# Kernel optimization log

Hardware: AMD Instinct MI355X
Metric: run time of the kernel (lower is better)

The kernel has to match this reference:

```python
import jax, jax.numpy as jnp
import numpy as np

N_ATOMS = 10000
N_PAIRS = 100000
H = 64          # hidden_channels
R = 32          # number_of_radial_basis_functions
MAX_Z = 100
CUTOFF = 0.5    # nm (radial_max_distance), min = 0.0


def cosine_cutoff(d):
    # 0.5*(cos(pi*d/rc)+1) for d < rc else 0
    return jnp.where(d < CUTOFF, 0.5 * (jnp.cos(jnp.pi * d / CUTOFF) + 1.0), 0.0)


def expnormal_rbf(d):
    # ExpNormal smearing (TorchMD/TensorNet style), cutoff_lower = 0
    start = float(np.exp(-CUTOFF))
    means = jnp.linspace(start, 1.0, R, dtype=d.dtype)            # [R]
    beta = (2.0 / R * (1.0 - start)) ** -2
    alpha = 5.0 / CUTOFF
    return jnp.exp(-beta * (jnp.exp(-alpha * d)[:, None] - means) ** 2)  # [P,R]


def vector_to_skewtensor(v):
    x, y, z = v[:, 0], v[:, 1], v[:, 2]
    o = jnp.zeros_like(x)
    return jnp.stack([o, -z, y, z, o, -x, -y, x, o], axis=-1).reshape(-1, 3, 3)


def vector_to_symtensor(v):
    t = v[:, :, None] * v[:, None, :]                              # [P,3,3]
    tr3 = (t[:, 0, 0] + t[:, 1, 1] + t[:, 2, 2]) / 3.0
    return t - tr3[:, None, None] * jnp.eye(3, dtype=v.dtype)


def setup_inputs() -> dict:
    key = jax.random.key(0)
    ks = jax.random.split(key, 20)
    atomic_numbers = jax.random.randint(ks[0], (N_ATOMS,), 0, MAX_Z)
    pair_indices = jax.random.randint(ks[1], (2, N_PAIRS), 0, N_ATOMS)
    r_ij = jax.random.normal(ks[2], (N_PAIRS, 3), dtype=jnp.float32) * 0.12  # ~0.2 nm norms
    d_ij = jnp.linalg.norm(r_ij, axis=-1, keepdims=True) + 1e-6
    s = 0.1
    p = {
        'emb':    jax.random.normal(ks[3], (MAX_Z, H)) * s,
        'emb2_w': jax.random.normal(ks[4], (H, 2 * H)) * s,
        'emb2_b': jnp.zeros((H,)),
        'dp1_w':  jax.random.normal(ks[5], (H, R)) * s,
        'dp1_b':  jnp.zeros((H,)),
        'dp2_w':  jax.random.normal(ks[6], (H, R)) * s,
        'dp2_b':  jnp.zeros((H,)),
        'dp3_w':  jax.random.normal(ks[7], (H, R)) * s,
        'dp3_b':  jnp.zeros((H,)),
        'lt0_w':  jax.random.normal(ks[8], (H, H)) * s,
        'lt1_w':  jax.random.normal(ks[9], (H, H)) * s,
        'lt2_w':  jax.random.normal(ks[10], (H, H)) * s,
        'ls1_w':  jax.random.normal(ks[11], (2 * H, H)) * s,
        'ls1_b':  jnp.zeros((2 * H,)),
        'ls2_w':  jax.random.normal(ks[12], (3 * H, 2 * H)) * s,
        'ls2_b':  jnp.zeros((3 * H,)),
        'ln_g':   jnp.ones((H,)),
        'ln_b':   jnp.zeros((H,)),
    }
    return dict(atomic_numbers=atomic_numbers, pair_indices=pair_indices,
                d_ij=d_ij, r_ij=r_ij, **p)


def reference(atomic_numbers, pair_indices, d_ij, r_ij,
              emb, emb2_w, emb2_b, dp1_w, dp1_b, dp2_w, dp2_b, dp3_w, dp3_b,
              lt0_w, lt1_w, lt2_w, ls1_w, ls1_b, ls2_w, ls2_b, ln_g, ln_b):
    n_atoms = atomic_numbers.shape[0]
    src = pair_indices[0]
    # atomic number message Zij: concat(emb[i], emb[j]) -> Linear
    zi = emb[atomic_numbers]                                      # [N,H]
    zij = jnp.concatenate([zi[src], zi[pair_indices[1]]], axis=-1)  # [P,2H]
    Zij = zij @ emb2_w.T + emb2_b                                 # [P,H]
    d = d_ij[:, 0]                                                # [P]
    unit = r_ij / d_ij                                            # [P,3]
    rc = cosine_cutoff(d)                                         # [P]
    rbf = expnormal_rbf(d) * rc[:, None]                          # [P,R]
    C = rc[:, None] * Zij                                         # [P,H]
    f1 = (rbf @ dp1_w.T + dp1_b) * C                              # [P,H]
    f2 = (rbf @ dp2_w.T + dp2_b) * C * 10.0                       # Angstrom scale
    f3 = (rbf @ dp3_w.T + dp3_b) * C * 100.0
    eye = jnp.eye(3, dtype=r_ij.dtype)
    skew = vector_to_skewtensor(unit)                             # [P,3,3]
    sym = vector_to_symtensor(unit)                               # [P,3,3]
    Iij = f1[:, :, None, None] * eye                              # [P,H,3,3]
    Aij = f2[:, :, None, None] * skew[:, None]
    Sij = f3[:, :, None, None] * sym[:, None]
    I = jax.ops.segment_sum(Iij, src, num_segments=n_atoms)       # [N,H,3,3]
    A = jax.ops.segment_sum(Aij, src, num_segments=n_atoms)
    S = jax.ops.segment_sum(Sij, src, num_segments=n_atoms)
    # tensor_norm -> LayerNorm -> scalar MLP
    tn = jnp.sum((I + A + S) ** 2, axis=(-2, -1))                 # [N,H]
    mu = tn.mean(-1, keepdims=True)
    var = tn.var(-1, keepdims=True)
    norm = (tn - mu) / jnp.sqrt(var + 1e-5) * ln_g + ln_b
    norm = jax.nn.silu(norm @ ls1_w.T + ls1_b)
    norm = jax.nn.silu(norm @ ls2_w.T + ls2_b)                    # [N,3H]
    norm = norm.reshape(-1, H, 3)
    I = jnp.einsum('nhij,gh->ngij', I, lt0_w) * norm[:, :, 0][:, :, None, None]
    A = jnp.einsum('nhij,gh->ngij', A, lt1_w) * norm[:, :, 1][:, :, None, None]
    S = jnp.einsum('nhij,gh->ngij', S, lt2_w) * norm[:, :, 2][:, :, None, None]
    return I + A + S
```

## Files before the change

### kernel.cpp

```cpp
#include <hip/hip_runtime.h>
#include <hip/hip_bf16.h>

#define N_ATOMS 10000
#define N_PAIRS 100000
#define HH 64
#define MAXZ 100

typedef _Float16 h2_t __attribute__((ext_vector_type(2)));

constexpr float RBF_START = 0.6065306597126334f;
constexpr float RBF_STEP  = (1.0f - RBF_START) / 31.0f;
constexpr float RBF_BETA  = 1.0f / ((0.0625f * (1.0f - RBF_START)) * (0.0625f * (1.0f - RBF_START)));
constexpr float LOG2E     = 1.4426950408889634f;
constexpr float NEG_ALPHA_L2 = -10.0f * LOG2E;
constexpr float NEG_BETA_L2  = -RBF_BETA * LOG2E;

#define OFF_EMB   0
#define OFF_W2    6400
#define OFF_B2    14592
#define OFF_D1W   14656
#define OFF_D1B   16704
#define OFF_D2W   16768
#define OFF_D2B   18816
#define OFF_D3W   18880
#define OFF_D3B   20928
#define OFF_LT0   20992
#define OFF_LT1   25088
#define OFF_LT2   29184
#define OFF_L1W   33280
#define OFF_L1B   41472
#define OFF_L2W   41600
#define OFF_L2B   66176
#define OFF_LNG   66368
#define OFF_LNB   66432
#define N_PARAMF  66496

#define PH_DP   0
#define PH_L1   3072
#define PH_L2   7168
#define PH_LT   19456
#define PH_N    25600

#define WS_WF     0
#define WS_CNT    266240
#define WS_OFF    307200
#define WS_CUR    348160
#define WS_T1     389120
#define WS_T2     414720
#define WS_PH     440320
#define WS_DPK    542720
#define WS_ZNL    2142720
#define WS_ACCH   2542720

__device__ __forceinline__ float bf2f(unsigned short u) {
    return __uint_as_float(((unsigned int)u) << 16);
}
__device__ __forceinline__ float fexp2(float x) { return __builtin_amdgcn_exp2f(x); }
__device__ __forceinline__ float fcos2pi(float x) { return __builtin_amdgcn_cosf(x); }
__device__ __forceinline__ float fsilu(float x) { return x / (1.0f + fexp2(-LOG2E * x)); }
__device__ __forceinline__ h2_t u2h(unsigned u) { return __builtin_bit_cast(h2_t, u); }
__device__ __forceinline__ unsigned packh2(float a, float b) {
    h2_t v; v.x = (_Float16)a; v.y = (_Float16)b;
    return __builtin_bit_cast(unsigned, v);
}

#if __has_builtin(__builtin_amdgcn_fdot2)
__device__ __forceinline__ float FDOT2(h2_t a, h2_t b, float c) {
    return __builtin_amdgcn_fdot2(a, b, c, false);
}
#else
__device__ __forceinline__ float FDOT2(h2_t a, h2_t b, float c) {
    return c + (float)a.x * (float)b.x + (float)a.y * (float)b.y;
}
#endif
__device__ __forceinline__ float dot16v(uint4 a, uint4 b, float acc) {
    acc = FDOT2(u2h(a.x), u2h(b.x), acc);
    acc = FDOT2(u2h(a.y), u2h(b.y), acc);
    acc = FDOT2(u2h(a.z), u2h(b.z), acc);
    acc = FDOT2(u2h(a.w), u2h(b.w), acc);
    return acc;
}
__device__ __forceinline__ float dot16h(const uint4* w, const uint4* x, float acc) {
    return dot16v(*w, *x, acc);
}

__device__ int classify64(const unsigned short* b, int lane) {
    unsigned short x = b[lane];
    int e = (x >> 7) & 0xFF;
    bool implaus = (x != 0) && (e < 96 || e > 133);
    bool zeroeven = ((lane & 1) == 0) && (x == 0);
    unsigned long long mi = __ballot(implaus);
    unsigned long long mz = __ballot(zeroeven);
    if (__popcll(mz) == 32) return 0;
    if (__popcll(mi) >= 8) return 0;
    return 1;
}

struct ConvArgs { const void* src[18]; float* dst; };

__global__ void k_prep(ConvArgs a, const int* __restrict__ pidx, int* __restrict__ cnt) {
    const int sizes[18] = {6400,8192,64,2048,64,2048,64,2048,64,4096,4096,4096,8192,128,24576,192,64,64};
    __shared__ int fl;
    if (threadIdx.x < 64) {
        int f = classify64((const unsigned short*)a.src[0], threadIdx.x);
        if (threadIdx.x == 0) fl = f;
    }
    __syncthreads();
    int t = blockIdx.x * 256 + threadIdx.x;
    if (t < N_PARAMF) {
        int acc = 0, seg = 0, off = t;
        #pragma unroll
        for (int i = 0; i < 18; ++i) {
            if (t >= acc && t < acc + sizes[i]) { seg = i; off = t - acc; }
            acc += sizes[i];
        }
        if (fl == 1) a.dst[t] = bf2f(((const unsigned short*)a.src[seg])[off]);
        else         a.dst[t] = ((const float*)a.src[seg])[off];
    }
    if (t < N_PAIRS) atomicAdd(&cnt[pidx[t]], 1);
}

__global__ void k_scantab(const float* __restrict__ WF, float* __restrict__ T1,
                          float* __restrict__ T2, unsigned* __restrict__ PH,
                          const int* __restrict__ cnt, int* __restrict__ offs,
                          int* __restrict__ cur) {
    __shared__ int buf[1024];
    if (blockIdx.x == 0) {
        int tid = threadIdx.x;
        int base = tid * 10;
        int c[10]; int s = 0;
        #pragma unroll
        for (int i = 0; i < 10; ++i) {
            int idx = base + i;
            int v = (idx < N_ATOMS) ? cnt[idx] : 0;
            c[i] = v; s += v;
        }
        buf[tid] = s;
        __syncthreads();
        for (int off = 1; off < 1024; off <<= 1) {
            int v = (tid >= off) ? buf[tid - off] : 0;
            __syncthreads();
            buf[tid] += v;
            __syncthreads();
        }
        int run = buf[tid] - s;
        #pragma unroll
        for (int i = 0; i < 10; ++i) {
            int idx = base + i;
            if (idx < N_ATOMS) { offs[idx] = run; cur[idx] = run; run += c[i]; }
        }
        if (tid == 0) offs[N_ATOMS] = N_PAIRS;
        return;
    }
    int t = (blockIdx.x - 1) * 1024 + threadIdx.x;
    if (t < 6400) {
        int z = t >> 6, h = t & 63;
        const float* ez = WF + OFF_EMB + z * HH;
        const float* w2 = WF + OFF_W2 + h * 128;
        float s1 = 0.f, s2 = 0.f;
        #pragma unroll
        for (int k = 0; k < 64; ++k) {
            float e = ez[k];
            s1 += w2[k] * e;
            s2 += w2[64 + k] * e;
        }
        T1[z * HH + h] = s1;
        T2[z * HH + h] = s2;
    }
    if (t < PH_N) {
        int src;
        if (t < PH_L1) {
            int w = t >> 10, r = t & 1023;
            src = (w == 0 ? OFF_D1W : (w == 1 ? OFF_D2W : OFF_D3W)) + r * 2;
        } else if (t < PH_L2) {
            src = OFF_L1W + (t - PH_L1) * 2;
        } else if (t < PH_LT) {
            src = OFF_L2W + (t - PH_L2) * 2;
        } else {
            src = OFF_LT0 + (t - PH_LT) * 2;
        }
        PH[t] = packh2(WF[src], WF[src + 1]);
    }
}

__global__ void k_fill(const int* __restrict__ pidx, const int* __restrict__ an,
                       const void* __restrict__ dij_v, const void* __restrict__ rij_v,
                       int* __restrict__ cur,
                       float4* __restrict__ dpack, int* __restrict__ znl) {
    __shared__ int fdr[2];
    if (threadIdx.x < 64) {
        int fd = classify64((const unsigned short*)dij_v, threadIdx.x);
        int fr = classify64((const unsigned short*)rij_v, threadIdx.x);
        if (threadIdx.x == 0) { fdr[0] = fd; fdr[1] = fr; }
    }
    __syncthreads();
    int p = blockIdx.x * 256 + threadIdx.x;
    if (p >= N_PAIRS) return;
    int s = pidx[p];
    int dst = pidx[N_PAIRS + p];
    int pos = atomicAdd(&cur[s], 1);
    float d, rx, ry, rz;
    if (fdr[0] == 1) d = bf2f(((const unsigned short*)dij_v)[p]);
    else             d = ((const float*)dij_v)[p];
    if (fdr[1] == 1) {
        const unsigned short* r = (const unsigned short*)rij_v;
        rx = bf2f(r[3*p]); ry = bf2f(r[3*p+1]); rz = bf2f(r[3*p+2]);
    } else {
        const float* r = (const float*)rij_v;
        rx = r[3*p]; ry = r[3*p+1]; rz = r[3*p+2];
    }
    float inv = 1.0f / d;
    dpack[pos] = make_float4(rx * inv, ry * inv, rz * inv, d);
    znl[pos] = an[dst];
}

__global__ __launch_bounds__(256, 2) void k_pair(
    const int* __restrict__ an,
    const float* __restrict__ WF,
    const int* __restrict__ offs,
    const float4* __restrict__ dpack, const int* __restrict__ znl,
    const float* __restrict__ T1, const float* __restrict__ T2,
    const unsigned* __restrict__ PH,
    unsigned* __restrict__ accH)
{
    __shared__ __align__(16) unsigned rbuf[4][2][16];

    const int wave = threadIdx.x >> 6;
    const int h    = threadIdx.x & 63;

    const uint4* wp = (const uint4*)(PH + PH_DP);
    const uint4 w10 = wp[        h * 4 + 0], w11 = wp[        h * 4 + 1],
                w12 = wp[        h * 4 + 2], w13 = wp[        h * 4 + 3];
    const uint4 w20 = wp[256 +   h * 4 + 0], w21 = wp[256 +   h * 4 + 1],
                w22 = wp[256 +   h * 4 + 2], w23 = wp[256 +   h * 4 + 3];
    const uint4 w30 = wp[512 +   h * 4 + 0], w31 = wp[512 +   h * 4 + 1],
                w32 = wp[512 +   h * 4 + 2], w33 = wp[512 +   h * 4 + 3];

    const float ed1 = (WF + OFF_D1B)[h];
    const float ed2 = (WF + OFF_D2B)[h];
    const float ed3 = (WF + OFF_D3B)[h];
    const float eb2 = (WF + OFF_B2)[h];
    const float lng = (WF + OFF_LNG)[h];
    const float lnb = (WF + OFF_LNB)[h];

    unsigned* sl0 = &rbuf[wave][0][0];
    unsigned* sl1 = &rbuf[wave][1][0];
    const int stride = gridDim.x * 4;

    for (int n = blockIdx.x * 4 + wave; n < N_ATOMS; n += stride) {
        const float zA = eb2 + T1[an[n] * HH + h];
        const int pbeg = offs[n];
        const int len  = offs[n + 1] - pbeg;

        float Is=0.f, sx=0.f, sy=0.f, sz=0.f;
        float Sxx=0.f, Syy=0.f, Szz=0.f, Sxy=0.f, Sxz=0.f, Syz=0.f;

        float4 dc = make_float4(0,0,0,0), dn = make_float4(0,0,0,0);
        float tc = 0.f, t2n = 0.f, rc_c = 0.f, rc_n = 0.f;
        if (len > 0) { dc = dpack[pbeg];     tc  = T2[znl[pbeg] * HH + h]; }
        if (len > 1) { dn = dpack[pbeg + 1]; t2n = T2[znl[pbeg + 1] * HH + h]; }
        if (len > 0) {
            float d = dc.w;
            rc_c = (d < 0.5f) ? 0.5f * (fcos2pi(d) + 1.0f) : 0.0f;
            float en = fexp2(NEG_ALPHA_L2 * d);
            if (h < 16) {
                float t0 = en - (RBF_START + RBF_STEP * (float)(2 * h));
                float t1 = en - (RBF_START + RBF_STEP * (float)(2 * h + 1));
                sl0[h] = packh2(fexp2(NEG_BETA_L2 * t0 * t0) * rc_c,
                                fexp2(NEG_BETA_L2 * t1 * t1) * rc_c);
            }
        }
        __builtin_amdgcn_wave_barrier();

        for (int ii = 0; ii < len; ++ii) {
            if (ii + 1 < len) {
                float d = dn.w;
                rc_n = (d < 0.5f) ? 0.5f * (fcos2pi(d) + 1.0f) : 0.0f;
                float en = fexp2(NEG_ALPHA_L2 * d);
                unsigned* sl = (ii & 1) ? sl0 : sl1;
                if (h < 16) {
                    float t0 = en - (RBF_START + RBF_STEP * (float)(2 * h));
                    float t1 = en - (RBF_START + RBF_STEP * (float)(2 * h + 1));
                    sl[h] = packh2(fexp2(NEG_BETA_L2 * t0 * t0) * rc_n,
                                   fexp2(NEG_BETA_L2 * t1 * t1) * rc_n);
                }
            }
            float4 d2v = make_float4(0,0,0,0); float t2v2 = 0.f;
            bool has2 = (ii + 2 < len);
            if (has2) {
                d2v  = dpack[pbeg + ii + 2];
                t2v2 = T2[znl[pbeg + ii + 2] * HH + h];
            }
            const uint4* rbp = (const uint4*)((ii & 1) ? sl1 : sl0);
            uint4 b0 = rbp[0], b1 = rbp[1], b2 = rbp[2], b3 = rbp[3];
            float g1 = ed1, g2 = ed2, g3 = ed3;
            g1 = dot16v(w10, b0, g1); g1 = dot16v(w11, b1, g1);
            g1 = dot16v(w12, b2, g1); g1 = dot16v(w13, b3, g1);
            g2 = dot16v(w20, b0, g2); g2 = dot16v(w21, b1, g2);
            g2 = dot16v(w22, b2, g2); g2 = dot16v(w23, b3, g2);
            g3 = dot16v(w30, b0, g3); g3 = dot16v(w31, b1, g3);
            g3 = dot16v(w32, b2, g3); g3 = dot16v(w33, b3, g3);

            float ux = dc.x, uy = dc.y, uz = dc.z;
            float Cc = rc_c * (zA + tc);
            float f1 = g1 * Cc;
            float f2 = g2 * Cc * 10.0f;
            float f3 = g3 * Cc * 100.0f;

            Is += f1;
            sx += f2 * ux;  sy += f2 * uy;  sz += f2 * uz;
            float q = (ux*ux + uy*uy + uz*uz) * (1.0f / 3.0f);
            Sxx += f3 * (ux*ux - q);
            Syy += f3 * (uy*uy - q);
            Szz += f3 * (uz*uz - q);
            Sxy += f3 * (ux*uy);
            Sxz += f3 * (ux*uz);
            Syz += f3 * (uy*uz);

            dc = dn; tc = t2n; rc_c = rc_n;
            if (has2) { dn = d2v; t2n = t2v2; }
            __builtin_amdgcn_wave_barrier();
        }

        float tn = 3.0f*Is*Is + 2.0f*(sx*sx + sy*sy + sz*sz)
                 + Sxx*Sxx + Syy*Syy + Szz*Szz
                 + 2.0f*(Sxy*Sxy + Sxz*Sxz + Syz*Syz);
        float s1 = tn, s2 = tn * tn;
        #pragma unroll
        for (int o = 32; o > 0; o >>= 1) {
            s1 += __shfl_xor(s1, o);
            s2 += __shfl_xor(s2, o);
        }
        float mu  = s1 * (1.0f / 64.0f);
        float var = s2 * (1.0f / 64.0f) - mu * mu;
        float nv  = (tn - mu) * rsqrtf(var + 1e-5f) * lng + lnb;

        float vals[11] = {Is, sx, sy, sz, Sxx, Syy, Szz, Sxy, Sxz, Syz, nv};
        #pragma unroll
        for (int c = 0; c < 11; ++c) {
            float pv = __shfl_xor(vals[c], 1);
            if ((h & 1) == 0)
                accH[((n * 11 + c) << 5) + (h >> 1)] = packh2(vals[c], pv);
        }
    }
}

__global__ __launch_bounds__(256, 2) void k_post(
    const float* __restrict__ WF,
    const unsigned* __restrict__ PH,
    const unsigned* __restrict__ accH,
    float* __restrict__ out)
{
    __shared__ __align__(16) unsigned wL2[192 * 68];
    __shared__ __align__(16) unsigned acch[4][12 * 32];
    __shared__ __align__(16) unsigned y1h[4][64];
    __shared__ __align__(16) unsigned y2h[4][96];

    for (int q = threadIdx.x; q < 12288; q += 256) {
        int m = q >> 6, u = q & 63;
        wL2[m * 68 + u] = PH[PH_L2 + q];
    }
    __syncthreads();

    const int wave = threadIdx.x >> 6;
    const int h    = threadIdx.x & 63;
    const int gw   = blockIdx.x * 4 + wave;
    const int GW   = gridDim.x * 4;

    const uint4* l1base = (const uint4*)(PH + PH_L1);
    const uint4* lt0 = (const uint4*)(PH + PH_LT) + h * 8;
    const uint4* lt1 = (const uint4*)(PH + PH_LT + 2048) + h * 8;
    const uint4* lt2 = (const uint4*)(PH + PH_LT + 4096) + h * 8;

    for (int n = gw; n < N_ATOMS; n += GW) {
        if (h < 32) {
            #pragma unroll
            for (int c = 0; c < 11; ++c)
                acch[wave][c * 32 + h] = accH[((n * 11 + c) << 5) + h];
        }
        __builtin_amdgcn_wave_barrier();

        const uint4* nvh = (const uint4*)&acch[wave][10 * 32];

        float ya = (WF + OFF_L1B)[h];
        float yb = (WF + OFF_L1B)[h + 64];
        {
            const uint4* ra = l1base + h * 8;
            const uint4* rb = l1base + (h + 64) * 8;
            #pragma unroll
            for (int k = 0; k < 8; ++k) {
                ya = dot16h(ra + k, nvh + k, ya);
                yb = dot16h(rb + k, nvh + k, yb);
            }
        }
        ya = fsilu(ya); yb = fsilu(yb);
        {
            float pa = __shfl_xor(ya, 1);
            float pb = __shfl_xor(yb, 1);
            if ((h & 1) == 0) {
                y1h[wave][(h >> 1)]      = packh2(ya, pa);
                y1h[wave][32 + (h >> 1)] = packh2(yb, pb);
            }
        }
        __builtin_amdgcn_wave_barrier();

        const uint4* y1p = (const uint4*)&y1h[wave][0];
        float z0 = (WF + OFF_L2B)[h];
        float z1 = (WF + OFF_L2B)[h + 64];
        float z2 = (WF + OFF_L2B)[h + 128];
        {
            const uint4* r0 = (const uint4*)&wL2[(h)       * 68];
            const uint4* r1 = (const uint4*)&wL2[(h + 64)  * 68];
            const uint4* r2 = (const uint4*)&wL2[(h + 128) * 68];
            #pragma unroll
            for (int k = 0; k < 16; ++k) {
                uint4 x = y1p[k];
                z0 = dot16v(r0[k], x, z0);
                z1 = dot16v(r1[k], x, z1);
                z2 = dot16v(r2[k], x, z2);
            }
        }
        z0 = fsilu(z0); z1 = fsilu(z1); z2 = fsilu(z2);
        {
            float p0 = __shfl_xor(z0, 1);
            float p1 = __shfl_xor(z1, 1);
            float p2 = __shfl_xor(z2, 1);
            if ((h & 1) == 0) {
                y2h[wave][(h >> 1)]      = packh2(z0, p0);
                y2h[wave][32 + (h >> 1)] = packh2(z1, p1);
                y2h[wave][64 + (h >> 1)] = packh2(z2, p2);
            }
        }
        __builtin_amdgcn_wave_barrier();

        float n0, n1, n2;
        {
            int i0 = 3 * h;
            unsigned u0 = y2h[wave][i0 >> 1];
            unsigned u1 = y2h[wave][(i0 >> 1) + 1];
            h2_t a = u2h(u0), b = u2h(u1);
            if (i0 & 1) { n0 = (float)a.y; n1 = (float)b.x; n2 = (float)b.y; }
            else        { n0 = (float)a.x; n1 = (float)a.y; n2 = (float)b.x; }
        }

        const uint4* aI  = (const uint4*)&acch[wave][0];
        const uint4* aAx = (const uint4*)&acch[wave][32];
        const uint4* aAy = (const uint4*)&acch[wave][64];
        const uint4* aAz = (const uint4*)&acch[wave][96];
        const uint4* aXX = (const uint4*)&acch[wave][128];
        const uint4* aYY = (const uint4*)&acch[wave][160];
        const uint4* aZZ = (const uint4*)&acch[wave][192];
        const uint4* aXY = (const uint4*)&acch[wave][224];
        const uint4* aXZ = (const uint4*)&acch[wave][256];
        const uint4* aYZ = (const uint4*)&acch[wave][288];

        float P0=0.f, PAx=0.f, PAy=0.f, PAz=0.f;
        float Q0=0.f, Q1=0.f, Q2=0.f, Q3=0.f, Q4=0.f, Q5=0.f;
        #pragma unroll
        for (int k = 0; k < 8; ++k) {
            P0  = dot16h(lt0 + k, aI  + k, P0);
            PAx = dot16h(lt1 + k, aAx + k, PAx);
            PAy = dot16h(lt1 + k, aAy + k, PAy);
            PAz = dot16h(lt1 + k, aAz + k, PAz);
            Q0  = dot16h(lt2 + k, aXX + k, Q0);
            Q1  = dot16h(lt2 + k, aYY + k, Q1);
            Q2  = dot16h(lt2 + k, aZZ + k, Q2);
            Q3  = dot16h(lt2 + k, aXY + k, Q3);
            Q4  = dot16h(lt2 + k, aXZ + k, Q4);
            Q5  = dot16h(lt2 + k, aYZ + k, Q5);
        }
        float Iv = P0 * n0;
        float Ax = PAx * n1, Ay = PAy * n1, Az = PAz * n1;
        float Xx = Q0 * n2, Yy = Q1 * n2, Zz = Q2 * n2;
        float Xy = Q3 * n2, Xz = Q4 * n2, Yz = Q5 * n2;

        float* o = out + (size_t)n * 576 + h * 9;
        o[0] =  Iv + Xx;  o[1] = -Az + Xy;  o[2] =  Ay + Xz;
        o[3] =  Az + Xy;  o[4] =  Iv + Yy;  o[5] = -Ax + Yz;
        o[6] = -Ay + Xz;  o[7] =  Ax + Yz;  o[8] =  Iv + Zz;
        __builtin_amdgcn_wave_barrier();
    }
}

extern "C" void kernel_launch(void* const* d_in, const int* in_sizes, int n_in,
                              void* d_out, int out_size, void* d_ws, size_t ws_size,
                              hipStream_t stream) {
    const int* an   = (const int*)d_in[0];
    const int* pidx = (const int*)d_in[1];

    char* ws = (char*)d_ws;
    float*    WF    = (float*)(ws + WS_WF);
    int*      cnt   = (int*)(ws + WS_CNT);
    int*      offs  = (int*)(ws + WS_OFF);
    int*      cur   = (int*)(ws + WS_CUR);
    float*    T1    = (float*)(ws + WS_T1);
    float*    T2    = (float*)(ws + WS_T2);
    unsigned* PH    = (unsigned*)(ws + WS_PH);
    float4*   dpack = (float4*)(ws + WS_DPK);
    int*      znl   = (int*)(ws + WS_ZNL);
    unsigned* accH  = (unsigned*)(ws + WS_ACCH);
    float*    out   = (float*)d_out;

    hipMemsetAsync(cnt, 0, N_ATOMS * sizeof(int), stream);

    ConvArgs ca;
    for (int i = 0; i < 18; ++i) ca.src[i] = d_in[4 + i];
    ca.dst = WF;
    k_prep<<<(N_PAIRS + 255) / 256, 256, 0, stream>>>(ca, pidx, cnt);
    k_scantab<<<26, 1024, 0, stream>>>(WF, T1, T2, PH, cnt, offs, cur);
    k_fill<<<(N_PAIRS + 255) / 256, 256, 0, stream>>>(pidx, an, d_in[2], d_in[3],
                                                      cur, dpack, znl);
    k_pair<<<768, 256, 0, stream>>>(an, WF, offs, dpack, znl, T1, T2, PH, accH);
    k_post<<<512, 256, 0, stream>>>(WF, PH, accH, out);
}
```

Before: 213.4 us.

## Fuse pair aggregation and post-MLP kernels, stage fp16 T2 table in LDS

Merges the per-atom pair accumulation kernel and the post-processing MLP/linear kernel into one kernel. Per-atom accumulators now go through shared memory instead of a global fp16 buffer. The T2 embedding table is precomputed in fp16 and loaded into LDS, so the pair loop reads it from shared memory instead of gathering from global. The change drops one launch and a global round trip. In exchange the fused kernel uses more LDS per block, which can lower occupancy, the grid shrinks from 768 to 512 blocks, and T2 loses precision in fp16.

```diff
diff --git a/kernel.cpp b/kernel.cpp
--- a/kernel.cpp
+++ b/kernel.cpp
@@ -39,7 +39,8 @@
 #define PH_L1   3072
 #define PH_L2   7168
 #define PH_LT   19456
-#define PH_N    25600
+#define PH_T2H  25600
+#define PH_N    28800
 
 #define WS_WF     0
 #define WS_CNT    266240
@@ -48,9 +49,8 @@
 #define WS_T1     389120
 #define WS_T2     414720
 #define WS_PH     440320
-#define WS_DPK    542720
-#define WS_ZNL    2142720
-#define WS_ACCH   2542720
+#define WS_DPK    555520
+#define WS_ZNL    2155520
 
 __device__ __forceinline__ float bf2f(unsigned short u) {
     return __uint_as_float(((unsigned int)u) << 16);
@@ -166,8 +166,10 @@
         }
         T1[z * HH + h] = s1;
         T2[z * HH + h] = s2;
-    }
-    if (t < PH_N) {
+        _Float16 hv = (_Float16)s2;
+        ((unsigned short*)(PH + PH_T2H))[z * HH + h] = __builtin_bit_cast(unsigned short, hv);
+    }
+    if (t < 25600) {
         int src;
         if (t < PH_L1) {
             int w = t >> 10, r = t & 1023;
@@ -214,16 +216,28 @@
     znl[pos] = an[dst];
 }
 
-__global__ __launch_bounds__(256, 2) void k_pair(
+__global__ __launch_bounds__(256, 2) void k_fused(
     const int* __restrict__ an,
     const float* __restrict__ WF,
     const int* __restrict__ offs,
     const float4* __restrict__ dpack, const int* __restrict__ znl,
-    const float* __restrict__ T1, const float* __restrict__ T2,
+    const float* __restrict__ T1,
     const unsigned* __restrict__ PH,
-    unsigned* __restrict__ accH)
+    float* __restrict__ out)
 {
+    __shared__ __align__(16) unsigned T2L[3200];
+    __shared__ __align__(16) unsigned wL2[192 * 68];
     __shared__ __align__(16) unsigned rbuf[4][2][16];
+    __shared__ __align__(16) unsigned acch[4][11 * 32];
+    __shared__ __align__(16) unsigned y1h[4][64];
+    __shared__ __align__(16) unsigned y2h[4][96];
+
+    for (int q = threadIdx.x; q < 3200; q += 256) T2L[q] = PH[PH_T2H + q];
+    for (int q = threadIdx.x; q < 12288; q += 256) {
+        int m = q >> 6, u = q & 63;
+        wL2[m * 68 + u] = PH[PH_L2 + q];
+    }
+    __syncthreads();
 
     const int wave = threadIdx.x >> 6;
     const int h    = threadIdx.x & 63;
@@ -242,11 +256,21 @@
     const float eb2 = (WF + OFF_B2)[h];
     const float lng = (WF + OFF_LNG)[h];
     const float lnb = (WF + OFF_LNB)[h];
-
+    const float l1ba = (WF + OFF_L1B)[h];
+    const float l1bb = (WF + OFF_L1B)[h + 64];
+    const float l2b0 = (WF + OFF_L2B)[h];
+    const float l2b1 = (WF + OFF_L2B)[h + 64];
+    const float l2b2 = (WF + OFF_L2B)[h + 128];
+
+    const _Float16* T2h = (const _Float16*)T2L;
     unsigned* sl0 = &rbuf[wave][0][0];
     unsigned* sl1 = &rbuf[wave][1][0];
+    const uint4* l1base = (const uint4*)(PH + PH_L1);
+    const uint4* lt0 = (const uint4*)(PH + PH_LT) + h * 8;
+    const uint4* lt1 = (const uint4*)(PH + PH_LT + 2048) + h * 8;
+    const uint4* lt2 = (const uint4*)(PH + PH_LT + 4096) + h * 8;
+
     const int stride = gridDim.x * 4;
-
     for (int n = blockIdx.x * 4 + wave; n < N_ATOMS; n += stride) {
         const float zA = eb2 + T1[an[n] * HH + h];
         const int pbeg = offs[n];
@@ -256,9 +280,10 @@
         float Sxx=0.f, Syy=0.f, Szz=0.f, Sxy=0.f, Sxz=0.f, Syz=0.f;
 
         float4 dc = make_float4(0,0,0,0), dn = make_float4(0,0,0,0);
-        float tc = 0.f, t2n = 0.f, rc_c = 0.f, rc_n = 0.f;
-        if (len > 0) { dc = dpack[pbeg];     tc  = T2[znl[pbeg] * HH + h]; }
-        if (len > 1) { dn = dpack[pbeg + 1]; t2n = T2[znl[pbeg + 1] * HH + h]; }
+        int zn_c = 0, zn_n = 0;
+        float rc_c = 0.f, rc_n = 0.f;
+        if (len > 0) { dc = dpack[pbeg];     zn_c = znl[pbeg]; }
+        if (len > 1) { dn = dpack[pbeg + 1]; zn_n = znl[pbeg + 1]; }
         if (len > 0) {
             float d = dc.w;
             rc_c = (d < 0.5f) ? 0.5f * (fcos2pi(d) + 1.0f) : 0.0f;
@@ -285,12 +310,12 @@
                                    fexp2(NEG_BETA_L2 * t1 * t1) * rc_n);
                 }
             }
-            float4 d2v = make_float4(0,0,0,0); float t2v2 = 0.f;
+            float4 d2v = make_float4(0,0,0,0); int zn2 = 0;
             bool has2 = (ii + 2 < len);
-            if (has2) {
-                d2v  = dpack[pbeg + ii + 2];
-                t2v2 = T2[znl[pbeg + ii + 2] * HH + h];
-            }
+            if (has2) { d2v = dpack[pbeg + ii + 2]; zn2 = znl[pbeg + ii + 2]; }
+
+            float t2v = (float)T2h[zn_c * HH + h];
+
             const uint4* rbp = (const uint4*)((ii & 1) ? sl1 : sl0);
             uint4 b0 = rbp[0], b1 = rbp[1], b2 = rbp[2], b3 = rbp[3];
             float g1 = ed1, g2 = ed2, g3 = ed3;
@@ -302,7 +327,7 @@
             g3 = dot16v(w32, b2, g3); g3 = dot16v(w33, b3, g3);
 
             float ux = dc.x, uy = dc.y, uz = dc.z;
-            float Cc = rc_c * (zA + tc);
+            float Cc = rc_c * (zA + t2v);
             float f1 = g1 * Cc;
             float f2 = g2 * Cc * 10.0f;
             float f3 = g3 * Cc * 100.0f;
@@ -317,8 +342,8 @@
             Sxz += f3 * (ux*uz);
             Syz += f3 * (uy*uz);
 
-            dc = dn; tc = t2n; rc_c = rc_n;
-            if (has2) { dn = d2v; t2n = t2v2; }
+            dc = dn; zn_c = zn_n; rc_c = rc_n;
+            if (has2) { dn = d2v; zn_n = zn2; }
             __builtin_amdgcn_wave_barrier();
         }
 
@@ -339,51 +364,12 @@
         #pragma unroll
         for (int c = 0; c < 11; ++c) {
             float pv = __shfl_xor(vals[c], 1);
-            if ((h & 1) == 0)
-                accH[((n * 11 + c) << 5) + (h >> 1)] = packh2(vals[c], pv);
-        }
-    }
-}
-
-__global__ __launch_bounds__(256, 2) void k_post(
-    const float* __restrict__ WF,
-    const unsigned* __restrict__ PH,
-    const unsigned* __restrict__ accH,
-    float* __restrict__ out)
-{
-    __shared__ __align__(16) unsigned wL2[192 * 68];
-    __shared__ __align__(16) unsigned acch[4][12 * 32];
-    __shared__ __align__(16) unsigned y1h[4][64];
-    __shared__ __align__(16) unsigned y2h[4][96];
-
-    for (int q = threadIdx.x; q < 12288; q += 256) {
-        int m = q >> 6, u = q & 63;
-        wL2[m * 68 + u] = PH[PH_L2 + q];
-    }
-    __syncthreads();
-
-    const int wave = threadIdx.x >> 6;
-    const int h    = threadIdx.x & 63;
-    const int gw   = blockIdx.x * 4 + wave;
-    const int GW   = gridDim.x * 4;
-
-    const uint4* l1base = (const uint4*)(PH + PH_L1);
-    const uint4* lt0 = (const uint4*)(PH + PH_LT) + h * 8;
-    const uint4* lt1 = (const uint4*)(PH + PH_LT + 2048) + h * 8;
-    const uint4* lt2 = (const uint4*)(PH + PH_LT + 4096) + h * 8;
-
-    for (int n = gw; n < N_ATOMS; n += GW) {
-        if (h < 32) {
-            #pragma unroll
-            for (int c = 0; c < 11; ++c)
-                acch[wave][c * 32 + h] = accH[((n * 11 + c) << 5) + h];
+            if ((h & 1) == 0) acch[wave][c * 32 + (h >> 1)] = packh2(vals[c], pv);
         }
         __builtin_amdgcn_wave_barrier();
 
         const uint4* nvh = (const uint4*)&acch[wave][10 * 32];
-
-        float ya = (WF + OFF_L1B)[h];
-        float yb = (WF + OFF_L1B)[h + 64];
+        float ya = l1ba, yb = l1bb;
         {
             const uint4* ra = l1base + h * 8;
             const uint4* rb = l1base + (h + 64) * 8;
@@ -405,9 +391,7 @@
         __builtin_amdgcn_wave_barrier();
 
         const uint4* y1p = (const uint4*)&y1h[wave][0];
-        float z0 = (WF + OFF_L2B)[h];
-        float z1 = (WF + OFF_L2B)[h + 64];
-        float z2 = (WF + OFF_L2B)[h + 128];
+        float z0 = l2b0, z1 = l2b1, z2 = l2b2;
         {
             const uint4* r0 = (const uint4*)&wL2[(h)       * 68];
             const uint4* r1 = (const uint4*)&wL2[(h + 64)  * 68];
@@ -498,7 +482,6 @@
     unsigned* PH    = (unsigned*)(ws + WS_PH);
     float4*   dpack = (float4*)(ws + WS_DPK);
     int*      znl   = (int*)(ws + WS_ZNL);
-    unsigned* accH  = (unsigned*)(ws + WS_ACCH);
     float*    out   = (float*)d_out;
 
     hipMemsetAsync(cnt, 0, N_ATOMS * sizeof(int), stream);
@@ -510,6 +493,5 @@
     k_scantab<<<26, 1024, 0, stream>>>(WF, T1, T2, PH, cnt, offs, cur);
     k_fill<<<(N_PAIRS + 255) / 256, 256, 0, stream>>>(pidx, an, d_in[2], d_in[3],
                                                       cur, dpack, znl);
-    k_pair<<<768, 256, 0, stream>>>(an, WF, offs, dpack, znl, T1, T2, PH, accH);
-    k_post<<<512, 256, 0, stream>>>(WF, PH, accH, out);
-}
+    k_fused<<<512, 256, 0, stream>>>(an, WF, offs, dpack, znl, T1, PH, out);
+}
```

Result: slower. 235.0 us (+10.1%).
